# Performance work log

Hardware: AMD Instinct MI355X
Metric: run time of the kernel (lower is better)

## Reference

```python
import jax, jax.numpy as jnp
import numpy as np

FEAT_DIM, M, K, D = 1024, 32, 256, 32
B = 8192
ALPHA = 1.0
BN_EPS = 1e-5
NORM_EPS = 1e-12  # F.normalize eps


def _l2_normalize(v, axis=-1):
    # matches torch F.normalize: v / max(||v||, eps)
    n = jnp.sqrt(jnp.sum(v * v, axis=axis, keepdims=True))
    return v / jnp.maximum(n, NORM_EPS)


def setup_inputs() -> dict:
    key = jax.random.key(0)
    kx, kc = jax.random.split(key)
    x = jax.random.normal(kx, (B, FEAT_DIM), dtype=jnp.float32)
    # xavier-uniform init over (M,K,D) then per-codeword L2 normalization (as in __init__)
    limit = float(np.sqrt(6.0 / (K + D)))
    C_k = jax.random.uniform(kc, (M, K, D), dtype=jnp.float32, minval=-limit, maxval=limit)
    C_k = _l2_normalize(C_k, axis=-1)
    return {"x": x, "C_k": C_k}


def reference(x, C_k):
    Bn = x.shape[0]
    x_ = x.reshape(Bn, M, D)                       # (B, M, D)
    x_norm_ = _l2_normalize(x_, axis=-1)           # per-subspace normalize
    x_normalized = x_norm_.reshape(Bn, FEAT_DIM)

    # per-subspace similarity: (B, M, K)
    sims = jnp.einsum('bmd,mkd->bmk', x_norm_, C_k)

    # BatchNorm1d(M, affine=False) in training mode: normalize per channel m over (B, K)
    mean = jnp.mean(sims, axis=(0, 2), keepdims=True)
    var = jnp.mean(jnp.square(sims - mean), axis=(0, 2), keepdims=True)  # biased var
    sims = (sims - mean) / jnp.sqrt(var + BN_EPS)

    # hard assignment + codeword gather (C_v == C_k in VQ mode)
    hard_codes = jnp.argmax(sims, axis=-1)                     # (B, M) int
    x_hat_hard_ = C_k[jnp.arange(M)[None, :], hard_codes]      # (B, M, D)
    x_hat_hard = x_hat_hard_.reshape(Bn, FEAT_DIM)

    # soft assignment (mask_topK is None)
    soft_codes = jax.nn.softmax(sims * ALPHA, axis=-1)         # (B, M, K)

    # straight-through: value = x_hat_hard, grad flows through x_normalized
    x_hat = x_normalized - jax.lax.stop_gradient(x_normalized - x_hat_hard)

    # pq_detach_opt == 'features'
    reg_loss = jnp.sum(jnp.square(jax.lax.stop_gradient(x_normalized) - x_hat_hard), axis=-1)  # (B,)

    return (x_hat, hard_codes, soft_codes, x_normalized, reg_loss)
```

## Files before the change

### kernel.cpp

```cpp
#include <hip/hip_runtime.h>
#include <cmath>

#define FEAT_DIM 1024
#define MM 32
#define KK 256
#define DD 32
#define BB 8192

constexpr float BN_EPS = 1e-5f;

typedef float f32x4  __attribute__((ext_vector_type(4)));
typedef float f32x16 __attribute__((ext_vector_type(16)));

__device__ __forceinline__ float wave_fsum(float v) {
    #pragma unroll
    for (int s = 32; s >= 1; s >>= 1) v += __shfl_xor(v, s);
    return v;
}

template <int CTRL, int RM = 0xf>
__device__ __forceinline__ float dppf(float v) {
    int r = __builtin_amdgcn_update_dpp(__builtin_bit_cast(int, v),
                                        __builtin_bit_cast(int, v),
                                        CTRL, RM, 0xf, false);
    return __builtin_bit_cast(float, r);
}
__device__ __forceinline__ float wave_dpp_max(float v) {
    v = fmaxf(v, dppf<0xB1>(v));
    v = fmaxf(v, dppf<0x4E>(v));
    v = fmaxf(v, dppf<0x141>(v));
    v = fmaxf(v, dppf<0x140>(v));
    v = fmaxf(v, dppf<0x142, 0xa>(v));
    v = fmaxf(v, dppf<0x143, 0xc>(v));
    return __builtin_bit_cast(float, __builtin_amdgcn_readlane(__builtin_bit_cast(int, v), 63));
}
__device__ __forceinline__ float wave_dpp_sum(float v) {
    v += dppf<0xB1>(v);
    v += dppf<0x4E>(v);
    v += dppf<0x141>(v);
    v += dppf<0x140>(v);
    v += dppf<0x142, 0xa>(v);
    v += dppf<0x143, 0xc>(v);
    return __builtin_bit_cast(float, __builtin_amdgcn_readlane(__builtin_bit_cast(int, v), 63));
}

__device__ __forceinline__ void sload_slice(f32x16& lo, f32x16& hi, const float* p) {
    asm volatile("s_load_dwordx16 %0, %2, 0x0\n\t"
                 "s_load_dwordx16 %1, %2, 0x40"
                 : "=s"(lo), "=s"(hi) : "s"(p));
}
__device__ __forceinline__ void swait(f32x16& lo, f32x16& hi) {
    asm volatile("s_waitcnt lgkmcnt(0)" : "+s"(lo), "+s"(hi));
    __builtin_amdgcn_sched_barrier(0);
}

__global__ void k_norm(const float* __restrict__ x, float* __restrict__ xn,
                       double* __restrict__ stats) {
    if (blockIdx.x == 0 && threadIdx.x < 2 * MM) stats[threadIdx.x] = 0.0;
    const int t = blockIdx.x * blockDim.x + threadIdx.x;
    float4 v = ((const float4*)x)[t];
    float ss = v.x*v.x + v.y*v.y + v.z*v.z + v.w*v.w;
    #pragma unroll
    for (int s = 1; s < 8; s <<= 1) ss += __shfl_xor(ss, s);
    const float r = 1.0f / fmaxf(sqrtf(ss), 1e-12f);
    float4 o = {v.x*r, v.y*r, v.z*r, v.w*r};
    ((float4*)xn)[t] = o;
}

__global__ void k_gram(const float* __restrict__ Ck, float* __restrict__ G,
                       float* __restrict__ S) {
    __shared__ float CT[DD][KK + 4];
    const int m = blockIdx.x, part = blockIdx.y;
    const int t = threadIdx.x, wid = t >> 6, lane = t & 63;
    const float4* cp = (const float4*)(Ck + ((size_t)m * KK + t) * DD);
    #pragma unroll
    for (int i = 0; i < 8; ++i) {
        float4 v = cp[i];
        CT[4*i+0][t] = v.x; CT[4*i+1][t] = v.y;
        CT[4*i+2][t] = v.z; CT[4*i+3][t] = v.w;
    }
    __syncthreads();
    #pragma unroll 1
    for (int ei = 0; ei < 32; ++ei) {
        const int e = part * 128 + wid * 32 + ei;
        const int i = e >> 5, j = e & 31;
        float acc = 0.f;
        #pragma unroll
        for (int c4 = 0; c4 < 4; ++c4)
            acc = fmaf(CT[i][lane + 64*c4], CT[j][lane + 64*c4], acc);
        acc = wave_fsum(acc);
        if (lane == 0) G[((size_t)m * DD + i) * DD + j] = acc;
    }
    if (part == 0 && wid == 0) {
        #pragma unroll 1
        for (int d = 0; d < DD; ++d) {
            float a = 0.f;
            #pragma unroll
            for (int c4 = 0; c4 < 4; ++c4) a += CT[d][lane + 64*c4];
            a = wave_fsum(a);
            if (lane == 0) S[m * DD + d] = a;
        }
    }
}

__global__ void k_stats2(const float* __restrict__ xn, const float* __restrict__ G,
                         const float* __restrict__ S, double* __restrict__ stats) {
    const int m = blockIdx.x;
    const int b = blockIdx.y * 256 + threadIdx.x;
    float xv[DD];
    {
        const float4* xp = (const float4*)(xn + (size_t)b * FEAT_DIM + m * DD);
        #pragma unroll
        for (int i = 0; i < 8; ++i) {
            float4 v = xp[i];
            xv[4*i+0]=v.x; xv[4*i+1]=v.y; xv[4*i+2]=v.z; xv[4*i+3]=v.w;
        }
    }
    const float4* Gp = (const float4*)(G + (size_t)m * DD * DD);
    const float*  Sp = S + m * DD;
    float q = 0.f, s = 0.f;
    #pragma unroll 4
    for (int i = 0; i < DD; ++i) {
        float y = 0.f;
        #pragma unroll
        for (int jv = 0; jv < 8; ++jv) {
            float4 g = Gp[i * 8 + jv];
            y = fmaf(g.x, xv[4*jv+0], y); y = fmaf(g.y, xv[4*jv+1], y);
            y = fmaf(g.z, xv[4*jv+2], y); y = fmaf(g.w, xv[4*jv+3], y);
        }
        q = fmaf(y, xv[i], q);
    }
    #pragma unroll
    for (int i = 0; i < DD; ++i) s = fmaf(Sp[i], xv[i], s);
    q = wave_fsum(q); s = wave_fsum(s);
    __shared__ float lq[4], ls[4];
    const int wid = threadIdx.x >> 6, lane = threadIdx.x & 63;
    if (lane == 0) { lq[wid] = q; ls[wid] = s; }
    __syncthreads();
    if (threadIdx.x == 0) {
        atomicAdd(&stats[2*m],   (double)((ls[0]+ls[1])+(ls[2]+ls[3])));
        atomicAdd(&stats[2*m+1], (double)((lq[0]+lq[1])+(lq[2]+lq[3])));
    }
}

template <int BT>
__global__ __launch_bounds__(256)
__attribute__((amdgpu_waves_per_eu(3, 3)))
void k_main(const float* __restrict__ xn, const float* __restrict__ Ck,
            const double* __restrict__ stats,
            float* __restrict__ xhat, float* __restrict__ hard,
            float* __restrict__ soft, float* __restrict__ part) {
    const int m = blockIdx.x;
    const int wid = threadIdx.x >> 6, lane = threadIdx.x & 63;

    const double Ninv = 1.0 / ((double)BB * (double)KK);
    const double mu  = stats[2*m] * Ninv;
    const double var = stats[2*m+1] * Ninv - mu * mu;
    const float rstd = (float)(1.0 / sqrt(var + (double)BN_EPS));
    const float c1 = rstd * 1.4426950408889634f;

    float c[4][DD];
    #pragma unroll
    for (int j = 0; j < 4; ++j) {
        const float4* cp = (const float4*)(Ck + ((size_t)m * KK + 4*lane + j) * DD);
        #pragma unroll
        for (int i = 0; i < 8; ++i) {
            float4 v = cp[i];
            c[j][4*i+0]=v.x; c[j][4*i+1]=v.y; c[j][4*i+2]=v.z; c[j][4*i+3]=v.w;
        }
    }

    const int b_base = blockIdx.y * (4 * BT) + wid;

    auto slice_ptr = [&](int it) {
        int b = b_base + 4 * it;
        b = min(b, BB - 1);
        const int bu = __builtin_amdgcn_readfirstlane(b);
        return xn + (size_t)bu * FEAT_DIM + m * DD;
    };

    auto process = [&](const f32x16& lo, const f32x16& hi, int b) {
        float d0=0.f, d1=0.f, d2=0.f, d3=0.f;
        #pragma unroll
        for (int i = 0; i < 4; ++i) {
            const float x0 = lo[4*i+0], x1 = lo[4*i+1], x2 = lo[4*i+2], x3 = lo[4*i+3];
            d0 = fmaf(x0, c[0][4*i+0], d0); d0 = fmaf(x1, c[0][4*i+1], d0);
            d0 = fmaf(x2, c[0][4*i+2], d0); d0 = fmaf(x3, c[0][4*i+3], d0);
            d1 = fmaf(x0, c[1][4*i+0], d1); d1 = fmaf(x1, c[1][4*i+1], d1);
            d1 = fmaf(x2, c[1][4*i+2], d1); d1 = fmaf(x3, c[1][4*i+3], d1);
            d2 = fmaf(x0, c[2][4*i+0], d2); d2 = fmaf(x1, c[2][4*i+1], d2);
            d2 = fmaf(x2, c[2][4*i+2], d2); d2 = fmaf(x3, c[2][4*i+3], d2);
            d3 = fmaf(x0, c[3][4*i+0], d3); d3 = fmaf(x1, c[3][4*i+1], d3);
            d3 = fmaf(x2, c[3][4*i+2], d3); d3 = fmaf(x3, c[3][4*i+3], d3);
        }
        #pragma unroll
        for (int i = 4; i < 8; ++i) {
            const int e = 4 * (i - 4);
            const float x0 = hi[e+0], x1 = hi[e+1], x2 = hi[e+2], x3 = hi[e+3];
            d0 = fmaf(x0, c[0][4*i+0], d0); d0 = fmaf(x1, c[0][4*i+1], d0);
            d0 = fmaf(x2, c[0][4*i+2], d0); d0 = fmaf(x3, c[0][4*i+3], d0);
            d1 = fmaf(x0, c[1][4*i+0], d1); d1 = fmaf(x1, c[1][4*i+1], d1);
            d1 = fmaf(x2, c[1][4*i+2], d1); d1 = fmaf(x3, c[1][4*i+3], d1);
            d2 = fmaf(x0, c[2][4*i+0], d2); d2 = fmaf(x1, c[2][4*i+1], d2);
            d2 = fmaf(x2, c[2][4*i+2], d2); d2 = fmaf(x3, c[2][4*i+3], d2);
            d3 = fmaf(x0, c[3][4*i+0], d3); d3 = fmaf(x1, c[3][4*i+1], d3);
            d3 = fmaf(x2, c[3][4*i+2], d3); d3 = fmaf(x3, c[3][4*i+3], d3);
        }

        const float p0 = exp2f(d0 * c1);
        const float p1 = exp2f(d1 * c1);
        const float p2 = exp2f(d2 * c1);
        const float p3 = exp2f(d3 * c1);

        const float mx = wave_dpp_max(fmaxf(fmaxf(d0, d1), fmaxf(d2, d3)));
        const unsigned long long m0 = __ballot(d0 == mx);
        const unsigned long long m1 = __ballot(d1 == mx);
        const unsigned long long m2 = __ballot(d2 == mx);
        const unsigned long long m3 = __ballot(d3 == mx);
        const int k0 = m0 ? 4*__builtin_ctzll(m0)+0 : 0x7fffffff;
        const int k1 = m1 ? 4*__builtin_ctzll(m1)+1 : 0x7fffffff;
        const int k2 = m2 ? 4*__builtin_ctzll(m2)+2 : 0x7fffffff;
        const int k3 = m3 ? 4*__builtin_ctzll(m3)+3 : 0x7fffffff;
        const int bi = min(min(k0, k1), min(k2, k3));

        const float tot = wave_dpp_sum((p0 + p1) + (p2 + p3));
        const float inv = __builtin_amdgcn_rcpf(tot);

        f32x4 o = {p0*inv, p1*inv, p2*inv, p3*inv};
        __builtin_nontemporal_store(o, (f32x4*)(soft + ((size_t)b * MM + m) * KK) + lane);
        if (lane == 0) {
            hard[(size_t)b * MM + m] = (float)bi;
            part[(size_t)m * BB + b] = 2.f - 2.f * mx;
        }
        if (lane < 8) {
            f32x4 cw = ((const f32x4*)(Ck + ((size_t)m * KK + bi) * DD))[lane];
            __builtin_nontemporal_store(cw, (f32x4*)(xhat + (size_t)b * FEAT_DIM + m * DD) + lane);
        }
    };

    f32x16 alo, ahi, blo, bhi;
    sload_slice(alo, ahi, slice_ptr(0));
    sload_slice(blo, bhi, slice_ptr(1));
    #pragma unroll 1
    for (int it = 0; it < BT; it += 2) {
        swait(alo, ahi);
        process(alo, ahi, b_base + 4 * it);
        sload_slice(alo, ahi, slice_ptr(it + 2));
        swait(blo, bhi);
        process(blo, bhi, b_base + 4 * (it + 1));
        sload_slice(blo, bhi, slice_ptr(it + 3));
    }
}

__global__ void k_regsum(const float* __restrict__ part, float* __restrict__ reg) {
    const int b = blockIdx.x * 256 + threadIdx.x;
    float a = 0.f;
    #pragma unroll
    for (int mm = 0; mm < MM; ++mm) a += part[(size_t)mm * BB + b];
    reg[b] = a;
}

extern "C" void kernel_launch(void* const* d_in, const int* in_sizes, int n_in,
                              void* d_out, int out_size, void* d_ws, size_t ws_size,
                              hipStream_t stream) {
    const float* x  = (const float*)d_in[0];
    const float* Ck = (const float*)d_in[1];

    float* out   = (float*)d_out;
    float* xhat  = out;
    float* hard  = xhat  + (size_t)BB * FEAT_DIM;
    float* soft  = hard  + (size_t)BB * MM;
    float* xnorm = soft  + (size_t)BB * MM * KK;
    float* reg   = xnorm + (size_t)BB * FEAT_DIM;

    double* stats = (double*)d_ws;
    float* partb  = (float*)d_ws + 256;
    float* Gbuf = soft;
    float* Sbuf = soft + (size_t)MM * DD * DD;

    k_norm<<<(BB * FEAT_DIM / 4) / 256, 256, 0, stream>>>(x, xnorm, stats);
    k_gram<<<dim3(MM, 8), 256, 0, stream>>>(Ck, Gbuf, Sbuf);
    k_stats2<<<dim3(MM, BB / 256), 256, 0, stream>>>(xnorm, Gbuf, Sbuf, stats);
    constexpr int BT = 32;
    k_main<BT><<<dim3(MM, BB / (4 * BT)), 256, 0, stream>>>(xnorm, Ck, stats, xhat, hard, soft, partb);
    k_regsum<<<BB / 256, 256, 0, stream>>>(partb, reg);
}
```

Baseline: 179.0 us.

## Split each row's codewords across the four waves with a shared-memory reduction

Before, each wave handled its own batch rows and each lane held four codewords (128 registers). Now all four waves of a block work on the same row: each lane holds one codeword, and per-wave max, argmax and sum are combined through shared memory behind a __syncthreads. The register cut allows higher occupancy (waves_per_eu raised to 6-8), and the grid becomes four times larger. The cost is a block barrier per row, fewer rows per block, and soft-output stores shrinking from 16 bytes to 4 bytes per lane.

```diff
diff --git a/kernel.cpp b/kernel.cpp
--- a/kernel.cpp
+++ b/kernel.cpp
@@ -145,13 +145,15 @@
 
 template <int BT>
 __global__ __launch_bounds__(256)
-__attribute__((amdgpu_waves_per_eu(3, 3)))
+__attribute__((amdgpu_waves_per_eu(6, 8)))
 void k_main(const float* __restrict__ xn, const float* __restrict__ Ck,
             const double* __restrict__ stats,
             float* __restrict__ xhat, float* __restrict__ hard,
             float* __restrict__ soft, float* __restrict__ part) {
+    __shared__ float exs[2][4][2];
+    __shared__ int   exi[2][4];
     const int m = blockIdx.x;
-    const int wid = threadIdx.x >> 6, lane = threadIdx.x & 63;
+    const int w = threadIdx.x >> 6, lane = threadIdx.x & 63;
 
     const double Ninv = 1.0 / ((double)BB * (double)KK);
     const double mu  = stats[2*m] * Ninv;
@@ -159,82 +161,65 @@
     const float rstd = (float)(1.0 / sqrt(var + (double)BN_EPS));
     const float c1 = rstd * 1.4426950408889634f;
 
-    float c[4][DD];
-    #pragma unroll
-    for (int j = 0; j < 4; ++j) {
-        const float4* cp = (const float4*)(Ck + ((size_t)m * KK + 4*lane + j) * DD);
-        #pragma unroll
-        for (int i = 0; i < 8; ++i) {
-            float4 v = cp[i];
-            c[j][4*i+0]=v.x; c[j][4*i+1]=v.y; c[j][4*i+2]=v.z; c[j][4*i+3]=v.w;
-        }
-    }
-
-    const int b_base = blockIdx.y * (4 * BT) + wid;
+    const int k = 64 * w + lane;
+    f32x4 cw[8];
+    {
+        const f32x4* cp = (const f32x4*)(Ck + ((size_t)m * KK + k) * DD);
+        #pragma unroll
+        for (int i = 0; i < 8; ++i) cw[i] = cp[i];
+    }
+
+    const int b0 = blockIdx.y * BT;
 
     auto slice_ptr = [&](int it) {
-        int b = b_base + 4 * it;
-        b = min(b, BB - 1);
-        const int bu = __builtin_amdgcn_readfirstlane(b);
-        return xn + (size_t)bu * FEAT_DIM + m * DD;
+        const int b = min(b0 + it, BB - 1);
+        return xn + (size_t)b * FEAT_DIM + m * DD;
     };
 
-    auto process = [&](const f32x16& lo, const f32x16& hi, int b) {
-        float d0=0.f, d1=0.f, d2=0.f, d3=0.f;
+    auto process = [&](const f32x16& lo, const f32x16& hi, int b, int par) {
+        float d = 0.f;
         #pragma unroll
         for (int i = 0; i < 4; ++i) {
-            const float x0 = lo[4*i+0], x1 = lo[4*i+1], x2 = lo[4*i+2], x3 = lo[4*i+3];
-            d0 = fmaf(x0, c[0][4*i+0], d0); d0 = fmaf(x1, c[0][4*i+1], d0);
-            d0 = fmaf(x2, c[0][4*i+2], d0); d0 = fmaf(x3, c[0][4*i+3], d0);
-            d1 = fmaf(x0, c[1][4*i+0], d1); d1 = fmaf(x1, c[1][4*i+1], d1);
-            d1 = fmaf(x2, c[1][4*i+2], d1); d1 = fmaf(x3, c[1][4*i+3], d1);
-            d2 = fmaf(x0, c[2][4*i+0], d2); d2 = fmaf(x1, c[2][4*i+1], d2);
-            d2 = fmaf(x2, c[2][4*i+2], d2); d2 = fmaf(x3, c[2][4*i+3], d2);
-            d3 = fmaf(x0, c[3][4*i+0], d3); d3 = fmaf(x1, c[3][4*i+1], d3);
-            d3 = fmaf(x2, c[3][4*i+2], d3); d3 = fmaf(x3, c[3][4*i+3], d3);
-        }
-        #pragma unroll
-        for (int i = 4; i < 8; ++i) {
-            const int e = 4 * (i - 4);
-            const float x0 = hi[e+0], x1 = hi[e+1], x2 = hi[e+2], x3 = hi[e+3];
-            d0 = fmaf(x0, c[0][4*i+0], d0); d0 = fmaf(x1, c[0][4*i+1], d0);
-            d0 = fmaf(x2, c[0][4*i+2], d0); d0 = fmaf(x3, c[0][4*i+3], d0);
-            d1 = fmaf(x0, c[1][4*i+0], d1); d1 = fmaf(x1, c[1][4*i+1], d1);
-            d1 = fmaf(x2, c[1][4*i+2], d1); d1 = fmaf(x3, c[1][4*i+3], d1);
-            d2 = fmaf(x0, c[2][4*i+0], d2); d2 = fmaf(x1, c[2][4*i+1], d2);
-            d2 = fmaf(x2, c[2][4*i+2], d2); d2 = fmaf(x3, c[2][4*i+3], d2);
-            d3 = fmaf(x0, c[3][4*i+0], d3); d3 = fmaf(x1, c[3][4*i+1], d3);
-            d3 = fmaf(x2, c[3][4*i+2], d3); d3 = fmaf(x3, c[3][4*i+3], d3);
-        }
-
-        const float p0 = exp2f(d0 * c1);
-        const float p1 = exp2f(d1 * c1);
-        const float p2 = exp2f(d2 * c1);
-        const float p3 = exp2f(d3 * c1);
-
-        const float mx = wave_dpp_max(fmaxf(fmaxf(d0, d1), fmaxf(d2, d3)));
-        const unsigned long long m0 = __ballot(d0 == mx);
-        const unsigned long long m1 = __ballot(d1 == mx);
-        const unsigned long long m2 = __ballot(d2 == mx);
-        const unsigned long long m3 = __ballot(d3 == mx);
-        const int k0 = m0 ? 4*__builtin_ctzll(m0)+0 : 0x7fffffff;
-        const int k1 = m1 ? 4*__builtin_ctzll(m1)+1 : 0x7fffffff;
-        const int k2 = m2 ? 4*__builtin_ctzll(m2)+2 : 0x7fffffff;
-        const int k3 = m3 ? 4*__builtin_ctzll(m3)+3 : 0x7fffffff;
-        const int bi = min(min(k0, k1), min(k2, k3));
-
-        const float tot = wave_dpp_sum((p0 + p1) + (p2 + p3));
-        const float inv = __builtin_amdgcn_rcpf(tot);
-
-        f32x4 o = {p0*inv, p1*inv, p2*inv, p3*inv};
-        __builtin_nontemporal_store(o, (f32x4*)(soft + ((size_t)b * MM + m) * KK) + lane);
-        if (lane == 0) {
-            hard[(size_t)b * MM + m] = (float)bi;
-            part[(size_t)m * BB + b] = 2.f - 2.f * mx;
-        }
-        if (lane < 8) {
-            f32x4 cw = ((const f32x4*)(Ck + ((size_t)m * KK + bi) * DD))[lane];
-            __builtin_nontemporal_store(cw, (f32x4*)(xhat + (size_t)b * FEAT_DIM + m * DD) + lane);
+            d = fmaf(lo[4*i+0], cw[i][0], d); d = fmaf(lo[4*i+1], cw[i][1], d);
+            d = fmaf(lo[4*i+2], cw[i][2], d); d = fmaf(lo[4*i+3], cw[i][3], d);
+        }
+        #pragma unroll
+        for (int i = 0; i < 4; ++i) {
+            d = fmaf(hi[4*i+0], cw[4+i][0], d); d = fmaf(hi[4*i+1], cw[4+i][1], d);
+            d = fmaf(hi[4*i+2], cw[4+i][2], d); d = fmaf(hi[4*i+3], cw[4+i][3], d);
+        }
+        const float p = exp2f(d * c1);
+
+        const float mxw = wave_dpp_max(d);
+        const unsigned long long mk = __ballot(d == mxw);
+        const int kiw = 64 * w + (int)__builtin_ctzll(mk);
+        const float totw = wave_dpp_sum(p);
+
+        if (lane == 0) { exs[par][w][0] = mxw; exs[par][w][1] = totw; exi[par][w] = kiw; }
+        __syncthreads();
+
+        float bmx = exs[par][0][0], btot = exs[par][0][1];
+        int bki = exi[par][0];
+        #pragma unroll
+        for (int w2 = 1; w2 < 4; ++w2) {
+            const float mx2 = exs[par][w2][0];
+            const int   ki2 = exi[par][w2];
+            if (mx2 > bmx) { bmx = mx2; bki = ki2; }
+            else if (mx2 == bmx && ki2 < bki) bki = ki2;
+            btot += exs[par][w2][1];
+        }
+        const float inv = __builtin_amdgcn_rcpf(btot);
+
+        __builtin_nontemporal_store(p * inv, soft + ((size_t)b * MM + m) * KK + k);
+        if (w == 0) {
+            if (lane == 0) {
+                hard[(size_t)b * MM + m] = (float)bki;
+                part[(size_t)m * BB + b] = 2.f - 2.f * bmx;
+            }
+            if (lane < 8) {
+                f32x4 cg = ((const f32x4*)(Ck + ((size_t)m * KK + bki) * DD))[lane];
+                __builtin_nontemporal_store(cg, (f32x4*)(xhat + (size_t)b * FEAT_DIM + m * DD) + lane);
+            }
         }
     };
 
@@ -244,10 +229,10 @@
     #pragma unroll 1
     for (int it = 0; it < BT; it += 2) {
         swait(alo, ahi);
-        process(alo, ahi, b_base + 4 * it);
+        process(alo, ahi, b0 + it, 0);
         sload_slice(alo, ahi, slice_ptr(it + 2));
         swait(blo, bhi);
-        process(blo, bhi, b_base + 4 * (it + 1));
+        process(blo, bhi, b0 + it + 1, 1);
         sload_slice(blo, bhi, slice_ptr(it + 3));
     }
 }
@@ -282,6 +267,6 @@
     k_gram<<<dim3(MM, 8), 256, 0, stream>>>(Ck, Gbuf, Sbuf);
     k_stats2<<<dim3(MM, BB / 256), 256, 0, stream>>>(xnorm, Gbuf, Sbuf, stats);
     constexpr int BT = 32;
-    k_main<BT><<<dim3(MM, BB / (4 * BT)), 256, 0, stream>>>(xnorm, Ck, stats, xhat, hard, soft, partb);
+    k_main<BT><<<dim3(MM, BB / BT), 256, 0, stream>>>(xnorm, Ck, stats, xhat, hard, soft, partb);
     k_regsum<<<BB / 256, 256, 0, stream>>>(partb, reg);
 }
```

After: 214.3 us. 19.7% more time.

## Fuse normalization into stats kernel and move xhat gather to post kernel

Applied to the files above, without the earlier changes.

Folds the L2 normalization into the stats kernel, which now reads raw x, writes xnorm, and rescales the quadratic and linear sums by the inverse norm. This removes a separate pass over x and xnorm. The xhat codeword gather moves out of the main kernel into a combined post kernel that also computes the reg sums. The main kernel gets a larger batch tile and a higher waves-per-EU target, which may cost registers or cause spills.

```diff
diff --git a/kernel.cpp b/kernel.cpp
--- a/kernel.cpp
+++ b/kernel.cpp
@@ -54,24 +54,12 @@
     __builtin_amdgcn_sched_barrier(0);
 }
 
-__global__ void k_norm(const float* __restrict__ x, float* __restrict__ xn,
-                       double* __restrict__ stats) {
-    if (blockIdx.x == 0 && threadIdx.x < 2 * MM) stats[threadIdx.x] = 0.0;
-    const int t = blockIdx.x * blockDim.x + threadIdx.x;
-    float4 v = ((const float4*)x)[t];
-    float ss = v.x*v.x + v.y*v.y + v.z*v.z + v.w*v.w;
-    #pragma unroll
-    for (int s = 1; s < 8; s <<= 1) ss += __shfl_xor(ss, s);
-    const float r = 1.0f / fmaxf(sqrtf(ss), 1e-12f);
-    float4 o = {v.x*r, v.y*r, v.z*r, v.w*r};
-    ((float4*)xn)[t] = o;
-}
-
 __global__ void k_gram(const float* __restrict__ Ck, float* __restrict__ G,
-                       float* __restrict__ S) {
+                       float* __restrict__ S, double* __restrict__ stats) {
     __shared__ float CT[DD][KK + 4];
     const int m = blockIdx.x, part = blockIdx.y;
     const int t = threadIdx.x, wid = t >> 6, lane = t & 63;
+    if (m == 0 && part == 0 && t < 2 * MM) stats[t] = 0.0;
     const float4* cp = (const float4*)(Ck + ((size_t)m * KK + t) * DD);
     #pragma unroll
     for (int i = 0; i < 8; ++i) {
@@ -103,17 +91,30 @@
     }
 }
 
-__global__ void k_stats2(const float* __restrict__ xn, const float* __restrict__ G,
-                         const float* __restrict__ S, double* __restrict__ stats) {
+__global__ void k_ns(const float* __restrict__ x, float* __restrict__ xn,
+                     const float* __restrict__ G, const float* __restrict__ S,
+                     double* __restrict__ stats) {
     const int m = blockIdx.x;
     const int b = blockIdx.y * 256 + threadIdx.x;
     float xv[DD];
     {
-        const float4* xp = (const float4*)(xn + (size_t)b * FEAT_DIM + m * DD);
+        const float4* xp = (const float4*)(x + (size_t)b * FEAT_DIM + m * DD);
         #pragma unroll
         for (int i = 0; i < 8; ++i) {
             float4 v = xp[i];
             xv[4*i+0]=v.x; xv[4*i+1]=v.y; xv[4*i+2]=v.z; xv[4*i+3]=v.w;
+        }
+    }
+    float ss = 0.f;
+    #pragma unroll
+    for (int i = 0; i < DD; ++i) ss = fmaf(xv[i], xv[i], ss);
+    const float rn = 1.0f / fmaxf(sqrtf(ss), 1e-12f);
+    {
+        float4* op = (float4*)(xn + (size_t)b * FEAT_DIM + m * DD);
+        #pragma unroll
+        for (int i = 0; i < 8; ++i) {
+            float4 o = {xv[4*i+0]*rn, xv[4*i+1]*rn, xv[4*i+2]*rn, xv[4*i+3]*rn};
+            op[i] = o;
         }
     }
     const float4* Gp = (const float4*)(G + (size_t)m * DD * DD);
@@ -132,6 +133,8 @@
     }
     #pragma unroll
     for (int i = 0; i < DD; ++i) s = fmaf(Sp[i], xv[i], s);
+    q = q * rn * rn;
+    s = s * rn;
     q = wave_fsum(q); s = wave_fsum(s);
     __shared__ float lq[4], ls[4];
     const int wid = threadIdx.x >> 6, lane = threadIdx.x & 63;
@@ -145,11 +148,11 @@
 
 template <int BT>
 __global__ __launch_bounds__(256)
-__attribute__((amdgpu_waves_per_eu(3, 3)))
+__attribute__((amdgpu_waves_per_eu(4, 4)))
 void k_main(const float* __restrict__ xn, const float* __restrict__ Ck,
             const double* __restrict__ stats,
-            float* __restrict__ xhat, float* __restrict__ hard,
-            float* __restrict__ soft, float* __restrict__ part) {
+            float* __restrict__ hard, float* __restrict__ soft,
+            float* __restrict__ part) {
     const int m = blockIdx.x;
     const int wid = threadIdx.x >> 6, lane = threadIdx.x & 63;
 
@@ -232,10 +235,6 @@
             hard[(size_t)b * MM + m] = (float)bi;
             part[(size_t)m * BB + b] = 2.f - 2.f * mx;
         }
-        if (lane < 8) {
-            f32x4 cw = ((const f32x4*)(Ck + ((size_t)m * KK + bi) * DD))[lane];
-            __builtin_nontemporal_store(cw, (f32x4*)(xhat + (size_t)b * FEAT_DIM + m * DD) + lane);
-        }
     };
 
     f32x16 alo, ahi, blo, bhi;
@@ -252,12 +251,24 @@
     }
 }
 
-__global__ void k_regsum(const float* __restrict__ part, float* __restrict__ reg) {
-    const int b = blockIdx.x * 256 + threadIdx.x;
-    float a = 0.f;
-    #pragma unroll
-    for (int mm = 0; mm < MM; ++mm) a += part[(size_t)mm * BB + b];
-    reg[b] = a;
+#define XHAT_BLOCKS ((BB * MM * 8) / 256)
+__global__ void k_post(const float* __restrict__ Ck, const float* __restrict__ hard,
+                       float* __restrict__ xhat, const float* __restrict__ part,
+                       float* __restrict__ reg) {
+    if (blockIdx.x < XHAT_BLOCKS) {
+        const int t = blockIdx.x * 256 + threadIdx.x;
+        const int i = t & 7, bm = t >> 3;
+        const int m = bm & (MM - 1);
+        const int k = (int)hard[bm];
+        f32x4 cw = ((const f32x4*)(Ck + ((size_t)m * KK + k) * DD))[i];
+        __builtin_nontemporal_store(cw, ((f32x4*)xhat) + (size_t)bm * 8 + i);
+    } else {
+        const int b = (blockIdx.x - XHAT_BLOCKS) * 256 + threadIdx.x;
+        float a = 0.f;
+        #pragma unroll
+        for (int mm = 0; mm < MM; ++mm) a += part[(size_t)mm * BB + b];
+        reg[b] = a;
+    }
 }
 
 extern "C" void kernel_launch(void* const* d_in, const int* in_sizes, int n_in,
@@ -278,10 +289,9 @@
     float* Gbuf = soft;
     float* Sbuf = soft + (size_t)MM * DD * DD;
 
-    k_norm<<<(BB * FEAT_DIM / 4) / 256, 256, 0, stream>>>(x, xnorm, stats);
-    k_gram<<<dim3(MM, 8), 256, 0, stream>>>(Ck, Gbuf, Sbuf);
-    k_stats2<<<dim3(MM, BB / 256), 256, 0, stream>>>(xnorm, Gbuf, Sbuf, stats);
-    constexpr int BT = 32;
-    k_main<BT><<<dim3(MM, BB / (4 * BT)), 256, 0, stream>>>(xnorm, Ck, stats, xhat, hard, soft, partb);
-    k_regsum<<<BB / 256, 256, 0, stream>>>(partb, reg);
-}
+    k_gram<<<dim3(MM, 8), 256, 0, stream>>>(Ck, Gbuf, Sbuf, stats);
+    k_ns<<<dim3(MM, BB / 256), 256, 0, stream>>>(x, xnorm, Gbuf, Sbuf, stats);
+    constexpr int BT = 64;
+    k_main<BT><<<dim3(MM, BB / (4 * BT)), 256, 0, stream>>>(xnorm, Ck, stats, hard, soft, partb);
+    k_post<<<XHAT_BLOCKS + BB / 256, 256, 0, stream>>>(Ck, hard, xhat, partb, reg);
+}
```

Result: slower. 257.5 us (+43.9%).
